# Kernel tuning notes

Measured on AMD Instinct MI355X. Metric: run time of the kernel, lower is better.

Reference implementation:

```python
import jax, jax.numpy as jnp
import numpy as np

V, E, H, D, A, P = 8000, 384, 512, 512, 512, 128
B, N = 16, 128
NEG = -1.0e9


def _lstm(x, Wih, Whh, b, reverse=False):
    # x: (B, T, E); torch gate order i, f, g, o
    Hd = Whh.shape[1]
    def step(carry, xt):
        h, c = carry
        gates = xt @ Wih.T + h @ Whh.T + b
        i, f, g, o = jnp.split(gates, 4, axis=-1)
        c = jax.nn.sigmoid(f) * c + jax.nn.sigmoid(i) * jnp.tanh(g)
        h = jax.nn.sigmoid(o) * jnp.tanh(c)
        return (h, c), h
    xs = jnp.swapaxes(x, 0, 1)
    if reverse:
        xs = xs[::-1]
    init = (jnp.zeros((x.shape[0], Hd), x.dtype), jnp.zeros((x.shape[0], Hd), x.dtype))
    _, hs = jax.lax.scan(step, init, xs)
    if reverse:
        hs = hs[::-1]
    return jnp.swapaxes(hs, 0, 1)


def _forward(src_ids, src_mask, confusionset_mask, emb, Wih_f, Whh_f, b_f, Wih_b, Whh_b, b_b,
             Wih_d, Whh_d, b_d, W1, W2, v_att, combine_W, combine_b, vocab_W, vocab_b,
             Wg_W, Wg_b, ptr_W, ptr_b, ps_W, ps_b):
    x = emb[src_ids]                                                     # (B,N,E)
    # bidirectional encoder
    enc_hs = jnp.concatenate([_lstm(x, Wih_f, Whh_f, b_f),
                              _lstm(x, Wih_b, Whh_b, b_b, reverse=True)], axis=-1)  # (B,N,2H)
    # decoder LSTMCell unrolled over max_len=N steps (teacher forcing on src chars)
    dec_h = _lstm(x, Wih_d, Whh_d, b_d)                                  # (B,N,D)
    # Bahdanau additive attention
    dterm = dec_h @ W1.T                                                 # (B,N,A)
    eterm = enc_hs @ W2.T                                                # (B,N,A)
    score = jnp.tanh(dterm[:, :, None, :] + eterm[:, None, :, :]) @ v_att  # (B,T,n)
    score = jnp.where(src_mask[:, None, :] == 0, NEG, score)
    alpha = jax.nn.softmax(score, axis=-1)
    context = jnp.einsum('btn,bnh->bth', alpha, enc_hs)                  # (B,T,2H)
    combined = jnp.tanh(jnp.concatenate([dec_h, context], axis=-1) @ combine_W.T + combine_b)  # (B,T,D)
    vocab_logits = combined @ vocab_W.T + vocab_b                        # (B,T,V)
    vocab_logits = jnp.where(confusionset_mask == 0, NEG, vocab_logits)
    # pointer logits: Locj = (t == j) indicator as extra feature
    loc = jnp.eye(N, dtype=combined.dtype)                               # (T,n)
    base = combined @ ptr_W[:, :D].T + ptr_b                             # (B,T,P)
    ph = jnp.tanh(base[:, :, None, :] + loc[None, :, :, None] * ptr_W[:, D][None, None, None, :])  # (B,T,n,P)
    pos_scores = ph @ ps_W + ps_b                                        # (B,T,n)
    sentinel = jnp.tanh(combined @ Wg_W.T + Wg_b).sum(-1, keepdims=True) # (B,T,1)
    pointer_logits = jnp.concatenate([pos_scores, sentinel], axis=-1)    # (B,T,n+1)
    pad_mask = jnp.concatenate([src_mask, jnp.ones((src_mask.shape[0], 1), src_mask.dtype)], axis=1)
    pointer_logits = jnp.where(pad_mask[:, None, :] == 0, NEG, pointer_logits)
    return pointer_logits, vocab_logits


def setup_inputs():
    ks = iter(jax.random.split(jax.random.key(0), 40))
    def g(shape, s=0.05):
        return jax.random.normal(next(ks), shape, jnp.float32) * s
    inp = {
        'src_ids': jax.random.randint(next(ks), (B, N), 1, V),
        'src_mask': jnp.ones((B, N), jnp.int32),
        'confusionset_mask': jax.random.randint(next(ks), (B, N, V), 0, 2).astype(jnp.int32),
        'emb': g((V, E)).at[0].set(0.0),  # padding_idx=0 row zeroed
        'Wih_f': g((4 * H, E)), 'Whh_f': g((4 * H, H)), 'b_f': g((4 * H,)),
        'Wih_b': g((4 * H, E)), 'Whh_b': g((4 * H, H)), 'b_b': g((4 * H,)),
        'Wih_d': g((4 * D, E)), 'Whh_d': g((4 * D, D)), 'b_d': g((4 * D,)),
        'W1': g((A, D)), 'W2': g((A, 2 * H)), 'v_att': g((A,)),
        'combine_W': g((D, D + 2 * H)), 'combine_b': g((D,)),
        'vocab_W': g((V, D)), 'vocab_b': g((V,)),
        'Wg_W': g((D, D)), 'Wg_b': g((D,)),
        'ptr_W': g((P, D + 1)), 'ptr_b': g((P,)),
        'ps_W': g((P,)), 'ps_b': g(()),
    }
    return inp


def reference(src_ids, src_mask, confusionset_mask, emb, Wih_f, Whh_f, b_f, Wih_b, Whh_b, b_b,
              Wih_d, Whh_d, b_d, W1, W2, v_att, combine_W, combine_b, vocab_W, vocab_b,
              Wg_W, Wg_b, ptr_W, ptr_b, ps_W, ps_b):
    return _forward(src_ids, src_mask, confusionset_mask, emb, Wih_f, Whh_f, b_f, Wih_b, Whh_b, b_b,
                    Wih_d, Whh_d, b_d, W1, W2, v_att, combine_W, combine_b, vocab_W, vocab_b,
                    Wg_W, Wg_b, ptr_W, ptr_b, ps_W, ps_b)
```

## Files before the change

kernel.cpp:

```cpp
#include <hip/hip_runtime.h>
#include <hip/hip_bf16.h>
#include <math.h>

#define NEGV -1000000000.0f

static constexpr int B_ = 16, N_ = 128, BN_ = 2048;
static constexpr int E_ = 384, V_ = 8000;

typedef __attribute__((ext_vector_type(8))) short short8v;
typedef __attribute__((ext_vector_type(4))) float f32x4;

__device__ inline float wave_sum(float v) {
#pragma unroll
  for (int o = 32; o; o >>= 1) v += __shfl_xor(v, o);
  return v;
}
__device__ inline float wave_max(float v) {
#pragma unroll
  for (int o = 32; o; o >>= 1) v = fmaxf(v, __shfl_xor(v, o));
  return v;
}
__device__ inline float fast_tanh(float x) {
  return 1.f - 2.f / (1.f + __expf(2.f * x));
}
__device__ inline float fast_tanh_pre(float x2) {
  return 1.f - 2.f / (1.f + __expf(x2));
}
__device__ inline float fast_sig(float x) {
  return 1.f / (1.f + __expf(-x));
}
__device__ __forceinline__ void gl16(const void* g, void* l) {
  __builtin_amdgcn_global_load_lds((const __attribute__((address_space(1))) void*)g,
                                   (__attribute__((address_space(3))) void*)l, 16, 0, 0);
}

__global__ __launch_bounds__(256) void embed_kernel(
    const int* __restrict__ ids, const float* __restrict__ emb,
    __hip_bfloat16* __restrict__ xb) {
  const int row = blockIdx.x;
  const int id = ids[row];
  for (int e = threadIdx.x; e < E_; e += 256)
    xb[(size_t)row * E_ + e] = __float2bfloat16(emb[(size_t)id * E_ + e]);
}

struct CastArgs {
  const float* s[12];
  unsigned long long d[12];
  int base[12];
  int total;
  int special;
};
__device__ inline void cast_body(const CastArgs& a, int gsize, int gid0) {
  const int nq = a.total >> 2;
  for (int q = gid0; q < nq; q += gsize) {
    const int e = q << 2;
    int k = 11;
    while (e < a.base[k]) --k;
    const int i = e - a.base[k];
    __hip_bfloat16* dst = (__hip_bfloat16*)a.d[k] + i;
    if (k == a.special) {
      const int row = i >> 9, col = i & 511;
      const float* sp = a.s[k] + (size_t)row * 513 + col;
#pragma unroll
      for (int u = 0; u < 4; ++u) dst[u] = __float2bfloat16(sp[u]);
    } else {
      float4 v = *(const float4*)(a.s[k] + i);
      __hip_bfloat16 h0 = __float2bfloat16(v.x), h1 = __float2bfloat16(v.y);
      __hip_bfloat16 h2 = __float2bfloat16(v.z), h3 = __float2bfloat16(v.w);
      ushort4 u4 = {*(unsigned short*)&h0, *(unsigned short*)&h1,
                    *(unsigned short*)&h2, *(unsigned short*)&h3};
      *(ushort4*)dst = u4;
    }
  }
}
__global__ __launch_bounds__(256) void cast_kernel(CastArgs a) {
  cast_body(a, gridDim.x * 256, blockIdx.x * 256 + threadIdx.x);
}

template <int ACT, bool MASK>
__global__ __launch_bounds__(256) void bgemm_kernel(
    const __hip_bfloat16* __restrict__ A, int lda,
    const __hip_bfloat16* __restrict__ W, int ldw,
    const float* __restrict__ bias,
    float* __restrict__ C, int ldc,
    __hip_bfloat16* __restrict__ Cb, int ldcb,
    int M, int N, int K,
    const int* __restrict__ mask, int ldm) {
  __shared__ __hip_bfloat16 Al[2][4096];
  __shared__ __hip_bfloat16 Bl[2][4096];
  const int tid = threadIdx.x;
  const int wid = tid >> 6, lane = tid & 63;
  const int m0 = blockIdx.y * 128, n0 = blockIdx.x * 128;
  const int nkt = K >> 5;
  const int rm = (wid >> 1) << 6, rn = (wid & 1) << 6;
  const int lrow = lane & 15, kq = lane >> 4;
  const int fs = ((lrow >> 1) & 3) << 4;

  f32x4 acc[4][4];
#pragma unroll
  for (int i = 0; i < 4; ++i)
#pragma unroll
    for (int j = 0; j < 4; ++j) acc[i][j] = {0.f, 0.f, 0.f, 0.f};

  auto stage = [&](int bi, int kt) {
#pragma unroll
    for (int c = 0; c < 2; ++c) {
      const int p = ((c * 4 + wid) << 6) + lane;
      const int row = p >> 2, cb = (p & 3) << 4;
      const int sw = ((row >> 1) & 3) << 4;
      const unsigned loff = (unsigned)__builtin_amdgcn_readfirstlane((c * 4 + wid) << 10);
      {
        const char* src = (const char*)A + ((size_t)(m0 + row) * lda + (size_t)kt * 32) * 2 + (cb ^ sw);
        gl16(src, (char*)&Al[bi][0] + loff);
      }
      {
        int gr = n0 + row;
        if (gr >= N) gr = N - 1;
        const char* src = (const char*)W + ((size_t)gr * ldw + (size_t)kt * 32) * 2 + (cb ^ sw);
        gl16(src, (char*)&Bl[bi][0] + loff);
      }
    }
  };
  auto compute = [&](int bi) {
    const char* Ab = (const char*)&Al[bi][0];
    const char* Bb = (const char*)&Bl[bi][0];
    const int roff = (kq << 4) ^ fs;
    short8v a[4], b[4];
#pragma unroll
    for (int i = 0; i < 4; ++i)
      a[i] = *(const short8v*)(Ab + (rm + i * 16 + lrow) * 64 + roff);
#pragma unroll
    for (int j = 0; j < 4; ++j)
      b[j] = *(const short8v*)(Bb + (rn + j * 16 + lrow) * 64 + roff);
#pragma unroll
    for (int i = 0; i < 4; ++i)
#pragma unroll
      for (int j = 0; j < 4; ++j)
        acc[i][j] = __builtin_amdgcn_mfma_f32_16x16x32_bf16(a[i], b[j], acc[i][j], 0, 0, 0);
  };

  stage(0, 0);
  for (int kt = 0; kt < nkt; ++kt) {
    __syncthreads();
    if (kt + 1 < nkt) stage((kt + 1) & 1, kt + 1);
    compute(kt & 1);
  }

#pragma unroll
  for (int i = 0; i < 4; ++i) {
#pragma unroll
    for (int r = 0; r < 4; ++r) {
      const int m = m0 + rm + i * 16 + kq * 4 + r;
#pragma unroll
      for (int j = 0; j < 4; ++j) {
        const int n = n0 + rn + j * 16 + lrow;
        if (n < N) {
          float v = acc[i][j][r] + (bias ? bias[n] : 0.f);
          if (ACT == 1) v = fast_tanh(v);
          if (MASK) {
            if (mask[(size_t)m * ldm + n] == 0) v = NEGV;
          }
          if (C) C[(size_t)m * ldc + n] = v;
          if (Cb) Cb[(size_t)m * ldcb + n] = __float2bfloat16(v);
        }
      }
    }
  }
}

template <int ACT, int TROUT>
__global__ __launch_bounds__(256) void bgemm64_kernel(
    const __hip_bfloat16* __restrict__ A, int lda,
    const __hip_bfloat16* __restrict__ W, int ldw,
    const float* __restrict__ bias, const float* __restrict__ bias2,
    float* __restrict__ C, int ldc, float* __restrict__ C2,
    __hip_bfloat16* __restrict__ Cb, int ldcb,
    int M, int N, int K,
    long aBs, long wBs, long cBs) {
  __shared__ __hip_bfloat16 Al[2][2048];
  __shared__ __hip_bfloat16 Bl[2][2048];
  A += (size_t)blockIdx.z * aBs;
  W += (size_t)blockIdx.z * wBs;
  const int tid = threadIdx.x;
  const int wid = tid >> 6, lane = tid & 63;
  const int m0 = blockIdx.y * 64, n0 = blockIdx.x * 64;
  const int nkt = K >> 5;
  const int rm = (wid >> 1) << 5, rn = (wid & 1) << 5;
  const int lrow = lane & 15, kq = lane >> 4;
  const int fs = ((lrow >> 1) & 3) << 4;

  f32x4 acc[2][2];
#pragma unroll
  for (int i = 0; i < 2; ++i)
#pragma unroll
    for (int j = 0; j < 2; ++j) acc[i][j] = {0.f, 0.f, 0.f, 0.f};

  auto stage = [&](int bi, int kt) {
    const int p = tid;
    const int row = p >> 2, cb = (p & 3) << 4;
    const int sw = ((row >> 1) & 3) << 4;
    const unsigned loff = (unsigned)__builtin_amdgcn_readfirstlane(wid << 10);
    {
      const char* src = (const char*)A + ((size_t)(m0 + row) * lda + (size_t)kt * 32) * 2 + (cb ^ sw);
      gl16(src, (char*)&Al[bi][0] + loff);
    }
    {
      const char* src = (const char*)W + ((size_t)(n0 + row) * ldw + (size_t)kt * 32) * 2 + (cb ^ sw);
      gl16(src, (char*)&Bl[bi][0] + loff);
    }
  };
  auto compute = [&](int bi) {
    const char* Ab = (const char*)&Al[bi][0];
    const char* Bb = (const char*)&Bl[bi][0];
    const int roff = (kq << 4) ^ fs;
    short8v a[2], b[2];
#pragma unroll
    for (int i = 0; i < 2; ++i)
      a[i] = *(const short8v*)(Ab + (rm + i * 16 + lrow) * 64 + roff);
#pragma unroll
    for (int j = 0; j < 2; ++j)
      b[j] = *(const short8v*)(Bb + (rn + j * 16 + lrow) * 64 + roff);
#pragma unroll
    for (int i = 0; i < 2; ++i)
#pragma unroll
      for (int j = 0; j < 2; ++j)
        acc[i][j] = __builtin_amdgcn_mfma_f32_16x16x32_bf16(a[i], b[j], acc[i][j], 0, 0, 0);
  };

  stage(0, 0);
  for (int kt = 0; kt < nkt; ++kt) {
    __syncthreads();
    if (kt + 1 < nkt) stage((kt + 1) & 1, kt + 1);
    compute(kt & 1);
  }

#pragma unroll
  for (int i = 0; i < 2; ++i) {
#pragma unroll
    for (int r = 0; r < 4; ++r) {
      const int m = m0 + rm + i * 16 + kq * 4 + r;
#pragma unroll
      for (int j = 0; j < 2; ++j) {
        const int n = n0 + rn + j * 16 + lrow;
        float v = acc[i][j][r];
        if (TROUT == 2) {
          if (n < 512) {
            C[(size_t)m * ldc + n] = fast_tanh(v + bias[n]);
          } else {
            C2[(size_t)m * 128 + (n - 512)] = v + bias2[n - 512];
          }
        } else {
          if (ACT == 2) v *= 2.f;
          else {
            v += (bias ? bias[n] : 0.f);
            if (ACT == 1) v = fast_tanh(v);
          }
          if (TROUT == 1) {
            Cb[(((size_t)(m >> 7) * 512 + n) << 7) + (m & 127)] = __float2bfloat16(v);
          } else {
            if (C) C[(size_t)m * ldc + n] = v;
            if (Cb) Cb[(size_t)m * ldcb + n + (size_t)blockIdx.z * cBs] = __float2bfloat16(v);
          }
        }
      }
    }
  }
}

__global__ __launch_bounds__(256) void fused_kernel(
    const __hip_bfloat16* __restrict__ xp16,
    const float* __restrict__ whhF, const float* __restrict__ whhB,
    const float* __restrict__ whhD,
    __hip_bfloat16* __restrict__ hbuf,
    __hip_bfloat16* __restrict__ ehsb, __hip_bfloat16* __restrict__ ehsT,
    __hip_bfloat16* __restrict__ catb,
    CastArgs ca2) {
  extern __shared__ char sm[];
  const int bid = blockIdx.x;
  const int tid = threadIdx.x;

  if (bid >= 96) {
    cast_body(ca2, 64 * 256, (bid - 96) * 256 + tid);
    return;
  }

  const int l = bid >> 5, g = bid & 31;
  const int lane = tid & 63, wid = tid >> 6;
  char* smW = sm;
  char* smH = sm + 65536;
  __hip_bfloat16* hout = (__hip_bfloat16*)(sm + 65536 + 16384);
  char* hist = sm + 65536 + 16384 + 512;

  const float* wsrc = (l == 0) ? whhF : ((l == 1) ? whhB : whhD);
  auto cv = [](float x) -> unsigned {
    __hip_bfloat16 h = __float2bfloat16(x);
    return (unsigned)*(unsigned short*)&h;
  };
  for (int p = tid; p < 4096; p += 256) {
    const int r = p >> 6, cb = (p & 63) << 4;
    const int grow = (r & 3) * 512 + (g << 4) + (r >> 2);
    const float* srcp = wsrc + (size_t)grow * 512 + ((p & 63) << 3);
    float4 u0 = *(const float4*)srcp;
    float4 u1 = *(const float4*)(srcp + 4);
    uint4 q;
    q.x = cv(u0.x) | (cv(u0.y) << 16);
    q.y = cv(u0.z) | (cv(u0.w) << 16);
    q.z = cv(u1.x) | (cv(u1.y) << 16);
    q.w = cv(u1.z) | (cv(u1.w) << 16);
    *(uint4*)(smW + r * 1024 + (cb ^ ((r & 7) << 4))) = q;
  }

  const int lrow = lane & 15, kq = lane >> 4;
  const int swz = (lrow & 7) << 4;
  const char* aB = smW + (wid * 16 + lrow) * 1024;
  const char* bB = smH + lrow * 1024;
  const int dl16 = wid * 4 + kq;
  const int dg = (g << 4) + dl16;
  const int bb = lrow;
  const bool rev = (l == 1);
  const __hip_bfloat16* xl = xp16 + (size_t)l * 2048 * 2048;
  __hip_bfloat16* hb_l = hbuf + (size_t)l * 128 * 8192;
  const int gq = tid >> 3;
  const int b0 = (tid & 7) * 2;
  const int gb = gq * 32;
  const int sw0 = (b0 & 7) << 4, sw1 = ((b0 + 1) & 7) << 4;
  float c = 0.f;

  for (int s = 0; s < 128; ++s) {
    const int t = rev ? 127 - s : s;
    const size_t xro = (size_t)(bb * 128 + t) * 2048 + dg;
    const float xgi = __bfloat162float(xl[xro]);
    const float xgf = __bfloat162float(xl[xro + 512]);
    const float xgg = __bfloat162float(xl[xro + 1024]);
    const float xgo = __bfloat162float(xl[xro + 1536]);

    if (s > 0) {
      if (gq != g) {
        const char* hsrc = (const char*)(hb_l + (size_t)(s - 1) * 8192);
        const unsigned loff = (unsigned)(tid * 64);
        unsigned hv;
        while (true) {
          asm volatile(
              "global_load_ushort %0, %1, %2 sc0 sc1\n\t"
              "s_waitcnt vmcnt(0)"
              : "=&v"(hv) : "v"(loff), "s"(hsrc) : "memory");
          if ((hv & 0xffffu) != 0x7f7fu) break;
          __builtin_amdgcn_s_sleep(1);
        }
        f32x4 q0, q1, q2, q3;
        asm volatile(
            "global_load_dwordx4 %0, %4, %5 sc0 sc1\n\t"
            "global_load_dwordx4 %1, %4, %5 offset:16 sc0 sc1\n\t"
            "global_load_dwordx4 %2, %4, %5 offset:32 sc0 sc1\n\t"
            "global_load_dwordx4 %3, %4, %5 offset:48 sc0 sc1\n\t"
            "s_waitcnt vmcnt(0)"
            : "=&v"(q0), "=&v"(q1), "=&v"(q2), "=&v"(q3)
            : "v"(loff), "s"(hsrc) : "memory");
        *(f32x4*)(smH + b0 * 1024 + (gb ^ sw0)) = q0;
        *(f32x4*)(smH + b0 * 1024 + ((gb + 16) ^ sw0)) = q1;
        *(f32x4*)(smH + (b0 + 1) * 1024 + (gb ^ sw1)) = q2;
        *(f32x4*)(smH + (b0 + 1) * 1024 + ((gb + 16) ^ sw1)) = q3;
      } else {
        const char* hl = (const char*)hout + b0 * 32;
        f32x4 c0 = *(const f32x4*)(hl);
        f32x4 c1 = *(const f32x4*)(hl + 16);
        f32x4 c2 = *(const f32x4*)(hl + 32);
        f32x4 c3 = *(const f32x4*)(hl + 48);
        *(f32x4*)(smH + b0 * 1024 + (gb ^ sw0)) = c0;
        *(f32x4*)(smH + b0 * 1024 + ((gb + 16) ^ sw0)) = c1;
        *(f32x4*)(smH + (b0 + 1) * 1024 + (gb ^ sw1)) = c2;
        *(f32x4*)(smH + (b0 + 1) * 1024 + ((gb + 16) ^ sw1)) = c3;
      }
    } else {
      const f32x4 z = {0.f, 0.f, 0.f, 0.f};
      *(f32x4*)(smH + b0 * 1024 + (gb ^ sw0)) = z;
      *(f32x4*)(smH + b0 * 1024 + ((gb + 16) ^ sw0)) = z;
      *(f32x4*)(smH + (b0 + 1) * 1024 + (gb ^ sw1)) = z;
      *(f32x4*)(smH + (b0 + 1) * 1024 + ((gb + 16) ^ sw1)) = z;
    }
    __syncthreads();

    f32x4 acc0 = {0.f, 0.f, 0.f, 0.f}, acc1 = {0.f, 0.f, 0.f, 0.f};
#pragma unroll
    for (int kt = 0; kt < 16; kt += 2) {
      const int off0 = ((kt * 64 + (kq << 4)) ^ swz);
      const int off1 = (((kt + 1) * 64 + (kq << 4)) ^ swz);
      short8v a0 = *(const short8v*)(aB + off0);
      short8v b0v = *(const short8v*)(bB + off0);
      short8v a1 = *(const short8v*)(aB + off1);
      short8v b1v = *(const short8v*)(bB + off1);
      acc0 = __builtin_amdgcn_mfma_f32_16x16x32_bf16(a0, b0v, acc0, 0, 0, 0);
      acc1 = __builtin_amdgcn_mfma_f32_16x16x32_bf16(a1, b1v, acc1, 0, 0, 0);
    }
    const f32x4 acc = acc0 + acc1;

    const float gi = acc[0] + xgi;
    const float gf = acc[1] + xgf;
    const float gg = acc[2] + xgg;
    const float go = acc[3] + xgo;
    c = fmaf(fast_sig(gf), c, fast_sig(gi) * fast_tanh(gg));
    const float h = fast_sig(go) * fast_tanh(c);
    __hip_bfloat16 hb16 = __float2bfloat16(h);
    const unsigned short hraw = *(unsigned short*)&hb16;
    hout[bb * 16 + dl16] = hb16;
    *(unsigned short*)(hist + s * 512 + (bb * 16 + dl16) * 2) = hraw;
    __syncthreads();

    if (s < 127 && wid == (s & 3) && (lane < 32)) {
      f32x4 hv4 = *(const f32x4*)((const char*)hout + lane * 16);
      char* hdst = (char*)(hb_l + (size_t)s * 8192);
      asm volatile("global_store_dwordx4 %0, %1, %2 sc0 sc1"
                   :: "v"((unsigned)((g << 9) + lane * 16)), "v"(hv4), "s"(hdst)
                   : "memory");
    }
  }

  __syncthreads();
  const int bb2 = tid >> 4, lo2 = tid & 15;
  if (l < 2) {
    const int hoff = (bb2 * 16 + lo2) * 2;
    char* dstT = (char*)(ehsT + ((size_t)bb2 * 1024 + l * 512 + (g << 4) + lo2) * 128);
    for (int tc = 0; tc < 128; tc += 32) {
      unsigned v[16];
#pragma unroll
      for (int w = 0; w < 16; ++w) {
        const int t0 = tc + 2 * w;
        const int s0 = rev ? 127 - t0 : t0;
        const int s1 = rev ? 126 - t0 : t0 + 1;
        unsigned a = *(const unsigned short*)(hist + s0 * 512 + hoff);
        unsigned b2 = *(const unsigned short*)(hist + s1 * 512 + hoff);
        v[w] = a | (b2 << 16);
      }
#pragma unroll
      for (int q = 0; q < 4; ++q)
        *(uint4*)(dstT + tc * 2 + q * 16) =
            make_uint4(v[q * 4], v[q * 4 + 1], v[q * 4 + 2], v[q * 4 + 3]);
    }
    for (int k = 0; k < 8; ++k) {
      const int t = lo2 * 8 + k;
      const int s0 = rev ? 127 - t : t;
      const char* srcp = hist + s0 * 512 + bb2 * 32;
      uint4 ra = *(const uint4*)srcp;
      uint4 rb = *(const uint4*)(srcp + 16);
      char* dp = (char*)(ehsb + ((size_t)(bb2 * 128 + t)) * 1024 + l * 512 + (g << 4));
      *(uint4*)dp = ra;
      *(uint4*)(dp + 16) = rb;
    }
  } else {
    for (int k = 0; k < 8; ++k) {
      const int t = lo2 * 8 + k;
      const char* srcp = hist + t * 512 + bb2 * 32;
      uint4 ra = *(const uint4*)srcp;
      uint4 rb = *(const uint4*)(srcp + 16);
      char* dp = (char*)(catb + ((size_t)(bb2 * 128 + t)) * 1536 + (g << 4));
      *(uint4*)dp = ra;
      *(uint4*)(dp + 16) = rb;
    }
  }
}

__global__ __launch_bounds__(256) void score_kernel(
    const float* __restrict__ dterm, const __hip_bfloat16* __restrict__ etT,
    const float* __restrict__ v_att, const int* __restrict__ src_mask,
    __hip_bfloat16* __restrict__ alphab) {
  const int b = blockIdx.x >> 5, tg = blockIdx.x & 31;
  const int t0 = tg * 4;
  const int tid = threadIdx.x;
  __shared__ float dt[4][512], vs[512], red[4][4][128], al[4][128];
  for (int i = tid; i < 2048; i += 256)
    dt[i >> 9][i & 511] = dterm[((size_t)(b * 128 + t0 + (i >> 9))) * 512 + (i & 511)];
  vs[tid] = v_att[tid];
  vs[tid + 256] = v_att[256 + tid];
  __syncthreads();
  const int n0 = (tid & 63) << 1, ah = tid >> 6;
  {
    const __hip_bfloat16* ep = etT + (((size_t)b * 512 + ah * 128) << 7) + n0;
    const float* vp = vs + ah * 128;
    const float* dp0 = &dt[0][ah * 128];
    const float* dp1 = &dt[1][ah * 128];
    const float* dp2 = &dt[2][ah * 128];
    const float* dp3 = &dt[3][ah * 128];
    float p00 = 0, p01 = 0, p10 = 0, p11 = 0, p20 = 0, p21 = 0, p30 = 0, p31 = 0;
    for (int a = 0; a < 128; ++a) {
      const unsigned u = *(const unsigned*)(ep + ((size_t)a << 7));
      unsigned u0 = u << 16, u1 = u & 0xffff0000u;
      const float e0 = __builtin_bit_cast(float, u0);
      const float e1 = __builtin_bit_cast(float, u1);
      const float va = vp[a];
      p00 = fmaf(va, fast_tanh_pre(dp0[a] + e0), p00);
      p01 = fmaf(va, fast_tanh_pre(dp0[a] + e1), p01);
      p10 = fmaf(va, fast_tanh_pre(dp1[a] + e0), p10);
      p11 = fmaf(va, fast_tanh_pre(dp1[a] + e1), p11);
      p20 = fmaf(va, fast_tanh_pre(dp2[a] + e0), p20);
      p21 = fmaf(va, fast_tanh_pre(dp2[a] + e1), p21);
      p30 = fmaf(va, fast_tanh_pre(dp3[a] + e0), p30);
      p31 = fmaf(va, fast_tanh_pre(dp3[a] + e1), p31);
    }
    red[0][ah][n0] = p00; red[0][ah][n0 + 1] = p01;
    red[1][ah][n0] = p10; red[1][ah][n0 + 1] = p11;
    red[2][ah][n0] = p20; red[2][ah][n0 + 1] = p21;
    red[3][ah][n0] = p30; red[3][ah][n0 + 1] = p31;
  }
  __syncthreads();
#pragma unroll
  for (int tp = 0; tp < 2; ++tp) {
    const int tt = tp * 2 + (tid >> 7);
    const int n = tid & 127;
    float sc = red[tt][0][n] + red[tt][1][n] + red[tt][2][n] + red[tt][3][n];
    if (src_mask[b * 128 + n] == 0) sc = NEGV;
    al[tt][n] = sc;
  }
  __syncthreads();
  {
    const int tt = tid >> 6, lane = tid & 63;
    const float v0 = al[tt][lane], v1 = al[tt][lane + 64];
    const float m = wave_max(fmaxf(v0, v1));
    const float e0 = __expf(v0 - m), e1 = __expf(v1 - m);
    const float inv = 1.f / wave_sum(e0 + e1);
    __hip_bfloat16* ap = alphab + ((size_t)(b * 128 + t0 + tt)) * 128;
    ap[lane] = __float2bfloat16(e0 * inv);
    ap[lane + 64] = __float2bfloat16(e1 * inv);
  }
}

__global__ __launch_bounds__(256) void pointer_kernel(
    const float* __restrict__ base, const float* __restrict__ wgout,
    const float* __restrict__ ptr_W, const float* __restrict__ ps_W,
    const float* __restrict__ ps_b, const int* __restrict__ src_mask,
    float* __restrict__ out0) {
  const int bt = blockIdx.x;
  const int b = bt >> 7, t = bt & 127;
  const int tid = threadIdx.x;
  __shared__ float r0[4], r1[4], r2[4], fin[3];
  float off_p = 0.f, diag_p = 0.f, sent_p;
  if (tid < 128) {
    const float ba = base[(size_t)bt * 128 + tid];
    const float pw = ps_W[tid];
    off_p = tanhf(ba) * pw;
    diag_p = tanhf(ba + ptr_W[tid * 513 + 512]) * pw;
  }
  sent_p = wgout[(size_t)bt * 512 + tid] + wgout[(size_t)bt * 512 + 256 + tid];
  off_p = wave_sum(off_p);
  diag_p = wave_sum(diag_p);
  sent_p = wave_sum(sent_p);
  const int wid = tid >> 6, lane = tid & 63;
  if (lane == 0) { r0[wid] = off_p; r1[wid] = diag_p; r2[wid] = sent_p; }
  __syncthreads();
  if (tid == 0) {
    const float psb = ps_b[0];
    fin[0] = r0[0] + r0[1] + r0[2] + r0[3] + psb;
    fin[1] = r1[0] + r1[1] + r1[2] + r1[3] + psb;
    fin[2] = r2[0] + r2[1] + r2[2] + r2[3];
  }
  __syncthreads();
  const float s_off = fin[0], s_diag = fin[1], sent = fin[2];
  if (tid < 129) {
    float v;
    if (tid == 128) v = sent;
    else {
      v = (tid == t) ? s_diag : s_off;
      if (src_mask[b * 128 + tid] == 0) v = NEGV;
    }
    out0[(size_t)bt * 129 + tid] = v;
  }
}

extern "C" void kernel_launch(void* const* d_in, const int* in_sizes, int n_in,
                              void* d_out, int out_size, void* d_ws, size_t ws_size,
                              hipStream_t stream) {
  const int* src_ids   = (const int*)d_in[0];
  const int* src_mask  = (const int*)d_in[1];
  const int* cmask     = (const int*)d_in[2];
  const float* emb     = (const float*)d_in[3];
  const float* Wih_f   = (const float*)d_in[4];
  const float* Whh_f   = (const float*)d_in[5];
  const float* b_f     = (const float*)d_in[6];
  const float* Wih_b   = (const float*)d_in[7];
  const float* Whh_b   = (const float*)d_in[8];
  const float* b_b     = (const float*)d_in[9];
  const float* Wih_d   = (const float*)d_in[10];
  const float* Whh_d   = (const float*)d_in[11];
  const float* b_d     = (const float*)d_in[12];
  const float* W1      = (const float*)d_in[13];
  const float* W2      = (const float*)d_in[14];
  const float* v_att   = (const float*)d_in[15];
  const float* comb_W  = (const float*)d_in[16];
  const float* comb_b  = (const float*)d_in[17];
  const float* vocab_W = (const float*)d_in[18];
  const float* vocab_b = (const float*)d_in[19];
  const float* Wg_W    = (const float*)d_in[20];
  const float* Wg_b    = (const float*)d_in[21];
  const float* ptr_W   = (const float*)d_in[22];
  const float* ptr_b   = (const float*)d_in[23];
  const float* ps_W    = (const float*)d_in[24];
  const float* ps_b    = (const float*)d_in[25];
  (void)in_sizes; (void)n_in; (void)out_size; (void)ws_size;

  char* wsb = (char*)d_ws;
  size_t o = 0;
  auto alloc = [&](size_t bytes) { char* p = wsb + o; o = (o + bytes + 255) & ~(size_t)255; return p; };
  __hip_bfloat16* xb      = (__hip_bfloat16*)alloc((size_t)BN_ * E_ * 2);
  __hip_bfloat16* xproj16 = (__hip_bfloat16*)alloc((size_t)3 * BN_ * 2048 * 2);
  __hip_bfloat16* ehsb    = (__hip_bfloat16*)alloc((size_t)BN_ * 1024 * 2);
  __hip_bfloat16* ehsT    = (__hip_bfloat16*)alloc((size_t)16 * 1024 * 128 * 2);
  __hip_bfloat16* catb    = (__hip_bfloat16*)alloc((size_t)BN_ * 1536 * 2);
  float* dterm            = (float*)alloc((size_t)BN_ * 512 * 4);
  __hip_bfloat16* etT     = (__hip_bfloat16*)alloc((size_t)16 * 512 * 128 * 2);
  __hip_bfloat16* alphab  = (__hip_bfloat16*)alloc((size_t)BN_ * 128 * 2);
  __hip_bfloat16* combb   = (__hip_bfloat16*)alloc((size_t)BN_ * 512 * 2);
  float* wgout            = (float*)alloc((size_t)BN_ * 512 * 4);
  float* baseb            = (float*)alloc((size_t)BN_ * 128 * 4);
  __hip_bfloat16* hbuf    = (__hip_bfloat16*)alloc((size_t)3 * 128 * 8192 * 2);
  __hip_bfloat16* wihf16  = (__hip_bfloat16*)alloc((size_t)2048 * 384 * 2);
  __hip_bfloat16* wihb16  = (__hip_bfloat16*)alloc((size_t)2048 * 384 * 2);
  __hip_bfloat16* wihd16  = (__hip_bfloat16*)alloc((size_t)2048 * 384 * 2);
  __hip_bfloat16* w1_16   = (__hip_bfloat16*)alloc((size_t)512 * 512 * 2);
  __hip_bfloat16* w2_16   = (__hip_bfloat16*)alloc((size_t)512 * 1024 * 2);
  __hip_bfloat16* combw16 = (__hip_bfloat16*)alloc((size_t)512 * 1536 * 2);
  __hip_bfloat16* vocw16  = (__hip_bfloat16*)alloc((size_t)8000 * 512 * 2);
  __hip_bfloat16* wgw16   = (__hip_bfloat16*)alloc((size_t)512 * 512 * 2);
  __hip_bfloat16* ptrw16  = (__hip_bfloat16*)alloc((size_t)128 * 512 * 2);

  float* out0 = (float*)d_out;
  float* out1 = out0 + (size_t)BN_ * 129;

  hipError_t e0 = hipMemsetAsync(hbuf, 0x7f, (size_t)3 * 128 * 8192 * 2, stream);
  (void)e0;
  embed_kernel<<<BN_, 256, 0, stream>>>(src_ids, emb, xb);

  CastArgs c1;
  {
    const float* s3[3] = {Wih_f, Wih_b, Wih_d};
    __hip_bfloat16* d3[3] = {wihf16, wihb16, wihd16};
    int acc = 0;
    for (int k = 0; k < 3; ++k) {
      c1.s[k] = s3[k]; c1.d[k] = (unsigned long long)d3[k]; c1.base[k] = acc;
      acc += 2048 * 384;
    }
    for (int k = 3; k < 12; ++k) { c1.s[k] = nullptr; c1.d[k] = 0; c1.base[k] = 0x7fffffff; }
    c1.total = acc; c1.special = -1;
  }
  cast_kernel<<<1024, 256, 0, stream>>>(c1);

  bgemm_kernel<0, false><<<dim3(16, 16), 256, 0, stream>>>(
      xb, E_, wihf16, E_, b_f, nullptr, 0, xproj16, 2048, BN_, 2048, E_, nullptr, 0);
  bgemm_kernel<0, false><<<dim3(16, 16), 256, 0, stream>>>(
      xb, E_, wihb16, E_, b_b, nullptr, 0, xproj16 + (size_t)BN_ * 2048, 2048, BN_, 2048, E_, nullptr, 0);
  bgemm_kernel<0, false><<<dim3(16, 16), 256, 0, stream>>>(
      xb, E_, wihd16, E_, b_d, nullptr, 0, xproj16 + (size_t)2 * BN_ * 2048, 2048, BN_, 2048, E_, nullptr, 0);

  CastArgs c2;
  {
    const float* s6[6] = {W1, W2, comb_W, vocab_W, Wg_W, ptr_W};
    __hip_bfloat16* d6[6] = {w1_16, w2_16, combw16, vocw16, wgw16, ptrw16};
    int ns[6] = {512 * 512, 512 * 1024, 512 * 1536, 8000 * 512, 512 * 512, 128 * 512};
    int acc = 0;
    for (int k = 0; k < 6; ++k) {
      c2.s[k] = s6[k]; c2.d[k] = (unsigned long long)d6[k]; c2.base[k] = acc;
      acc += ns[k];
    }
    for (int k = 6; k < 12; ++k) { c2.s[k] = nullptr; c2.d[k] = 0; c2.base[k] = 0x7fffffff; }
    c2.total = acc; c2.special = 5;
  }

  hipError_t e1 = hipFuncSetAttribute((const void*)fused_kernel,
                      hipFuncAttributeMaxDynamicSharedMemorySize, 147968);
  (void)e1;
  fused_kernel<<<160, 256, 147968, stream>>>(
      xproj16, Whh_f, Whh_b, Whh_d, hbuf, ehsb, ehsT, catb, c2);

  bgemm64_kernel<2, 0><<<dim3(8, 32), 256, 0, stream>>>(
      catb, 1536, w1_16, 512, nullptr, nullptr, dterm, 512, nullptr, nullptr, 0,
      BN_, 512, 512, 0, 0, 0);
  bgemm64_kernel<2, 1><<<dim3(8, 32), 256, 0, stream>>>(
      ehsb, 1024, w2_16, 1024, nullptr, nullptr, nullptr, 0, nullptr, etT, 0,
      BN_, 512, 1024, 0, 0, 0);

  score_kernel<<<16 * 32, 256, 0, stream>>>(dterm, etT, v_att, src_mask, alphab);

  bgemm64_kernel<0, 0><<<dim3(16, 2, 16), 256, 0, stream>>>(
      alphab, 128, ehsT, 128, nullptr, nullptr, nullptr, 0, nullptr,
      catb + 512, 1536, 128, 1024, 128, 128 * 128, 1024 * 128, 128 * 1536);

  bgemm64_kernel<1, 0><<<dim3(8, 32), 256, 0, stream>>>(
      catb, 1536, combw16, 1536, comb_b, nullptr, nullptr, 0, nullptr,
      combb, 512, BN_, 512, 1536, 0, 0, 0);

  bgemm_kernel<0, true><<<dim3(63, 16), 256, 0, stream>>>(
      combb, 512, vocw16, 512, vocab_b, out1, V_, nullptr, 0, BN_, V_, 512, cmask, V_);

  bgemm64_kernel<0, 2><<<dim3(10, 32), 256, 0, stream>>>(
      combb, 512, wgw16, 512, Wg_b, ptr_b, wgout, 512, baseb, nullptr, 0,
      BN_, 640, 512, 0, 0, 0);

  pointer_kernel<<<BN_, 256, 0, stream>>>(baseb, wgout, ptr_W, ps_W, ps_b, src_mask, out0);
}
```

Baseline: 605.6 us.

## Merge prologue, projection and tail GEMM launches into fewer combined kernels

The memset of hbuf, the embedding gather and the Wih weight cast are folded into one prologue kernel that splits its work by block index. The memset becomes cache-bypassing stores of the 0x7f pattern. The three input-projection GEMMs become one launch with a z dimension. The two attention projection GEMMs are merged into one launch, and so are the vocab and Wg/pointer GEMMs, by dispatching on block id. The GEMM bodies are turned into device functions with runtime activation and output modes. This removes several kernel launches and the gaps between them, and lets independent GEMMs share one grid. The cost is some branching and fewer compile-time specialisations.

```diff
diff --git a/kernel.cpp b/kernel.cpp
--- a/kernel.cpp
+++ b/kernel.cpp
@@ -34,19 +34,10 @@
                                    (__attribute__((address_space(3))) void*)l, 16, 0, 0);
 }
 
-__global__ __launch_bounds__(256) void embed_kernel(
-    const int* __restrict__ ids, const float* __restrict__ emb,
-    __hip_bfloat16* __restrict__ xb) {
-  const int row = blockIdx.x;
-  const int id = ids[row];
-  for (int e = threadIdx.x; e < E_; e += 256)
-    xb[(size_t)row * E_ + e] = __float2bfloat16(emb[(size_t)id * E_ + e]);
-}
-
 struct CastArgs {
-  const float* s[12];
-  unsigned long long d[12];
-  int base[12];
+  const float* s[6];
+  unsigned long long d[6];
+  int base[6];
   int total;
   int special;
 };
@@ -54,7 +45,7 @@
   const int nq = a.total >> 2;
   for (int q = gid0; q < nq; q += gsize) {
     const int e = q << 2;
-    int k = 11;
+    int k = 5;
     while (e < a.base[k]) --k;
     const int i = e - a.base[k];
     __hip_bfloat16* dst = (__hip_bfloat16*)a.d[k] + i;
@@ -73,24 +64,41 @@
     }
   }
 }
-__global__ __launch_bounds__(256) void cast_kernel(CastArgs a) {
-  cast_body(a, gridDim.x * 256, blockIdx.x * 256 + threadIdx.x);
+
+__global__ __launch_bounds__(256) void prologue_kernel(
+    const int* __restrict__ ids, const float* __restrict__ emb,
+    __hip_bfloat16* __restrict__ xb, __hip_bfloat16* __restrict__ hbuf,
+    CastArgs c1) {
+  const int bid = blockIdx.x, tid = threadIdx.x;
+  if (bid < 256) {
+    for (int row = bid; row < 2048; row += 256) {
+      const int id = ids[row];
+      for (int e = tid; e < E_; e += 256)
+        xb[(size_t)row * E_ + e] = __float2bfloat16(emb[(size_t)id * E_ + e]);
+    }
+  } else if (bid < 288) {
+    const unsigned total = 3u * 128u * 8192u * 2u;
+    const float pf = __builtin_bit_cast(float, 0x7f7f7f7fu);
+    f32x4 pat = {pf, pf, pf, pf};
+    char* base = (char*)hbuf;
+    for (unsigned off = (unsigned)((bid - 256) * 256 + tid) * 16u; off < total;
+         off += 32u * 256u * 16u) {
+      asm volatile("global_store_dwordx4 %0, %1, %2 sc0 sc1"
+                   :: "v"(off), "v"(pat), "s"(base) : "memory");
+    }
+  } else {
+    cast_body(c1, 256 * 256, (bid - 288) * 256 + tid);
+  }
 }
 
 template <int ACT, bool MASK>
-__global__ __launch_bounds__(256) void bgemm_kernel(
-    const __hip_bfloat16* __restrict__ A, int lda,
-    const __hip_bfloat16* __restrict__ W, int ldw,
-    const float* __restrict__ bias,
-    float* __restrict__ C, int ldc,
-    __hip_bfloat16* __restrict__ Cb, int ldcb,
-    int M, int N, int K,
-    const int* __restrict__ mask, int ldm) {
-  __shared__ __hip_bfloat16 Al[2][4096];
-  __shared__ __hip_bfloat16 Bl[2][4096];
+__device__ __forceinline__ void gemm128_impl(
+    const __hip_bfloat16* A, int lda, const __hip_bfloat16* W, int ldw,
+    const float* bias, float* C, int ldc, __hip_bfloat16* Cb, int ldcb,
+    int N, int K, const int* mask, int ldm, int m0, int n0,
+    __hip_bfloat16 (*Al)[4096], __hip_bfloat16 (*Bl)[4096]) {
   const int tid = threadIdx.x;
   const int wid = tid >> 6, lane = tid & 63;
-  const int m0 = blockIdx.y * 128, n0 = blockIdx.x * 128;
   const int nkt = K >> 5;
   const int rm = (wid >> 1) << 6, rn = (wid & 1) << 6;
   const int lrow = lane & 15, kq = lane >> 4;
@@ -168,22 +176,13 @@
   }
 }
 
-template <int ACT, int TROUT>
-__global__ __launch_bounds__(256) void bgemm64_kernel(
-    const __hip_bfloat16* __restrict__ A, int lda,
-    const __hip_bfloat16* __restrict__ W, int ldw,
-    const float* __restrict__ bias, const float* __restrict__ bias2,
-    float* __restrict__ C, int ldc, float* __restrict__ C2,
-    __hip_bfloat16* __restrict__ Cb, int ldcb,
-    int M, int N, int K,
-    long aBs, long wBs, long cBs) {
-  __shared__ __hip_bfloat16 Al[2][2048];
-  __shared__ __hip_bfloat16 Bl[2][2048];
-  A += (size_t)blockIdx.z * aBs;
-  W += (size_t)blockIdx.z * wBs;
+__device__ __forceinline__ void gemm64_impl(
+    const __hip_bfloat16* A, int lda, const __hip_bfloat16* W, int ldw,
+    const float* bias, const float* bias2,
+    float* C, int ldc, float* C2, __hip_bfloat16* Cb, int ldcb,
+    int K, int act, int trout, int m0, int n0, char* AlB, char* BlB) {
   const int tid = threadIdx.x;
   const int wid = tid >> 6, lane = tid & 63;
-  const int m0 = blockIdx.y * 64, n0 = blockIdx.x * 64;
   const int nkt = K >> 5;
   const int rm = (wid >> 1) << 5, rn = (wid & 1) << 5;
   const int lrow = lane & 15, kq = lane >> 4;
@@ -196,22 +195,21 @@
     for (int j = 0; j < 2; ++j) acc[i][j] = {0.f, 0.f, 0.f, 0.f};
 
   auto stage = [&](int bi, int kt) {
-    const int p = tid;
-    const int row = p >> 2, cb = (p & 3) << 4;
+    const int row = tid >> 2, cb = (tid & 3) << 4;
     const int sw = ((row >> 1) & 3) << 4;
     const unsigned loff = (unsigned)__builtin_amdgcn_readfirstlane(wid << 10);
     {
       const char* src = (const char*)A + ((size_t)(m0 + row) * lda + (size_t)kt * 32) * 2 + (cb ^ sw);
-      gl16(src, (char*)&Al[bi][0] + loff);
+      gl16(src, AlB + bi * 4096 + loff);
     }
     {
       const char* src = (const char*)W + ((size_t)(n0 + row) * ldw + (size_t)kt * 32) * 2 + (cb ^ sw);
-      gl16(src, (char*)&Bl[bi][0] + loff);
+      gl16(src, BlB + bi * 4096 + loff);
     }
   };
   auto compute = [&](int bi) {
-    const char* Ab = (const char*)&Al[bi][0];
-    const char* Bb = (const char*)&Bl[bi][0];
+    const char* Ab = AlB + bi * 4096;
+    const char* Bb = BlB + bi * 4096;
     const int roff = (kq << 4) ^ fs;
     short8v a[2], b[2];
 #pragma unroll
@@ -243,27 +241,98 @@
       for (int j = 0; j < 2; ++j) {
         const int n = n0 + rn + j * 16 + lrow;
         float v = acc[i][j][r];
-        if (TROUT == 2) {
+        if (trout == 2) {
           if (n < 512) {
             C[(size_t)m * ldc + n] = fast_tanh(v + bias[n]);
           } else {
             C2[(size_t)m * 128 + (n - 512)] = v + bias2[n - 512];
           }
         } else {
-          if (ACT == 2) v *= 2.f;
+          if (act == 2) v *= 2.f;
           else {
             v += (bias ? bias[n] : 0.f);
-            if (ACT == 1) v = fast_tanh(v);
+            if (act == 1) v = fast_tanh(v);
           }
-          if (TROUT == 1) {
+          if (trout == 1) {
             Cb[(((size_t)(m >> 7) * 512 + n) << 7) + (m & 127)] = __float2bfloat16(v);
           } else {
             if (C) C[(size_t)m * ldc + n] = v;
-            if (Cb) Cb[(size_t)m * ldcb + n + (size_t)blockIdx.z * cBs] = __float2bfloat16(v);
+            if (Cb) Cb[(size_t)m * ldcb + n] = __float2bfloat16(v);
           }
         }
       }
     }
+  }
+}
+
+__global__ __launch_bounds__(256) void xproj_kernel(
+    const __hip_bfloat16* __restrict__ A, const __hip_bfloat16* __restrict__ Wih,
+    const float* __restrict__ b0, const float* __restrict__ b1,
+    const float* __restrict__ b2, __hip_bfloat16* __restrict__ xproj16) {
+  __shared__ __hip_bfloat16 Al[2][4096], Bl[2][4096];
+  const int z = blockIdx.z;
+  const float* bias = (z == 0) ? b0 : (z == 1 ? b1 : b2);
+  gemm128_impl<0, false>(A, E_, Wih + (size_t)z * 2048 * 384, E_, bias,
+                         nullptr, 0, xproj16 + (size_t)z * BN_ * 2048, 2048,
+                         2048, E_, nullptr, 0, blockIdx.y * 128,
+                         blockIdx.x * 128, Al, Bl);
+}
+
+__global__ __launch_bounds__(256) void qk_kernel(
+    const __hip_bfloat16* __restrict__ catb, const __hip_bfloat16* __restrict__ ehsb,
+    const __hip_bfloat16* __restrict__ w1, const __hip_bfloat16* __restrict__ w2,
+    float* __restrict__ dterm, __hip_bfloat16* __restrict__ etT) {
+  __shared__ char AlB[8192], BlB[8192];
+  const int bid = blockIdx.x;
+  if (bid < 256) {
+    const int bx = bid & 7, by = bid >> 3;
+    gemm64_impl(catb, 1536, w1, 512, nullptr, nullptr, dterm, 512, nullptr,
+                nullptr, 0, 512, 2, 0, by * 64, bx * 64, AlB, BlB);
+  } else {
+    const int l = bid - 256;
+    const int bx = l & 7, by = l >> 3;
+    gemm64_impl(ehsb, 1024, w2, 1024, nullptr, nullptr, nullptr, 0, nullptr,
+                etT, 0, 1024, 2, 1, by * 64, bx * 64, AlB, BlB);
+  }
+}
+
+__global__ __launch_bounds__(256) void ctx_kernel(
+    const __hip_bfloat16* __restrict__ alphab, const __hip_bfloat16* __restrict__ ehsT,
+    __hip_bfloat16* __restrict__ catbCtx) {
+  __shared__ char AlB[8192], BlB[8192];
+  const int z = blockIdx.z;
+  gemm64_impl(alphab + (size_t)z * 128 * 128, 128,
+              ehsT + (size_t)z * 1024 * 128, 128, nullptr, nullptr, nullptr, 0,
+              nullptr, catbCtx + (size_t)z * 128 * 1536, 1536, 128, 0, 0,
+              blockIdx.y * 64, blockIdx.x * 64, AlB, BlB);
+}
+
+__global__ __launch_bounds__(256) void comb_kernel(
+    const __hip_bfloat16* __restrict__ catb, const __hip_bfloat16* __restrict__ combw,
+    const float* __restrict__ comb_b, __hip_bfloat16* __restrict__ combb) {
+  __shared__ char AlB[8192], BlB[8192];
+  gemm64_impl(catb, 1536, combw, 1536, comb_b, nullptr, nullptr, 0, nullptr,
+              combb, 512, 1536, 1, 0, blockIdx.y * 64, blockIdx.x * 64, AlB, BlB);
+}
+
+__global__ __launch_bounds__(256) void tail_kernel(
+    const __hip_bfloat16* __restrict__ combb, const __hip_bfloat16* __restrict__ vocw,
+    const float* __restrict__ vocab_b, float* __restrict__ out1,
+    const int* __restrict__ cmask,
+    const __hip_bfloat16* __restrict__ wgw, const float* __restrict__ Wg_b,
+    const float* __restrict__ ptr_b, float* __restrict__ wgout,
+    float* __restrict__ baseb) {
+  __shared__ __hip_bfloat16 Al[2][4096], Bl[2][4096];
+  const int bid = blockIdx.x;
+  if (bid < 1008) {
+    const int bx = bid % 63, by = bid / 63;
+    gemm128_impl<0, true>(combb, 512, vocw, 512, vocab_b, out1, V_, nullptr, 0,
+                          V_, 512, cmask, V_, by * 128, bx * 128, Al, Bl);
+  } else {
+    const int l = bid - 1008;
+    const int bx = l % 10, by = l / 10;
+    gemm64_impl(combb, 512, wgw, 512, Wg_b, ptr_b, wgout, 512, baseb, nullptr,
+                0, 512, 0, 2, by * 64, bx * 64, (char*)Al, (char*)Bl);
   }
 }
 
@@ -611,9 +680,7 @@
   float* wgout            = (float*)alloc((size_t)BN_ * 512 * 4);
   float* baseb            = (float*)alloc((size_t)BN_ * 128 * 4);
   __hip_bfloat16* hbuf    = (__hip_bfloat16*)alloc((size_t)3 * 128 * 8192 * 2);
-  __hip_bfloat16* wihf16  = (__hip_bfloat16*)alloc((size_t)2048 * 384 * 2);
-  __hip_bfloat16* wihb16  = (__hip_bfloat16*)alloc((size_t)2048 * 384 * 2);
-  __hip_bfloat16* wihd16  = (__hip_bfloat16*)alloc((size_t)2048 * 384 * 2);
+  __hip_bfloat16* wih16   = (__hip_bfloat16*)alloc((size_t)3 * 2048 * 384 * 2);
   __hip_bfloat16* w1_16   = (__hip_bfloat16*)alloc((size_t)512 * 512 * 2);
   __hip_bfloat16* w2_16   = (__hip_bfloat16*)alloc((size_t)512 * 1024 * 2);
   __hip_bfloat16* combw16 = (__hip_bfloat16*)alloc((size_t)512 * 1536 * 2);
@@ -624,31 +691,19 @@
   float* out0 = (float*)d_out;
   float* out1 = out0 + (size_t)BN_ * 129;
 
-  hipError_t e0 = hipMemsetAsync(hbuf, 0x7f, (size_t)3 * 128 * 8192 * 2, stream);
-  (void)e0;
-  embed_kernel<<<BN_, 256, 0, stream>>>(src_ids, emb, xb);
-
   CastArgs c1;
   {
     const float* s3[3] = {Wih_f, Wih_b, Wih_d};
-    __hip_bfloat16* d3[3] = {wihf16, wihb16, wihd16};
     int acc = 0;
     for (int k = 0; k < 3; ++k) {
-      c1.s[k] = s3[k]; c1.d[k] = (unsigned long long)d3[k]; c1.base[k] = acc;
+      c1.s[k] = s3[k];
+      c1.d[k] = (unsigned long long)(wih16 + (size_t)k * 2048 * 384);
+      c1.base[k] = acc;
       acc += 2048 * 384;
     }
-    for (int k = 3; k < 12; ++k) { c1.s[k] = nullptr; c1.d[k] = 0; c1.base[k] = 0x7fffffff; }
+    for (int k = 3; k < 6; ++k) { c1.s[k] = nullptr; c1.d[k] = 0; c1.base[k] = 0x7fffffff; }
     c1.total = acc; c1.special = -1;
   }
-  cast_kernel<<<1024, 256, 0, stream>>>(c1);
-
-  bgemm_kernel<0, false><<<dim3(16, 16), 256, 0, stream>>>(
-      xb, E_, wihf16, E_, b_f, nullptr, 0, xproj16, 2048, BN_, 2048, E_, nullptr, 0);
-  bgemm_kernel<0, false><<<dim3(16, 16), 256, 0, stream>>>(
-      xb, E_, wihb16, E_, b_b, nullptr, 0, xproj16 + (size_t)BN_ * 2048, 2048, BN_, 2048, E_, nullptr, 0);
-  bgemm_kernel<0, false><<<dim3(16, 16), 256, 0, stream>>>(
-      xb, E_, wihd16, E_, b_d, nullptr, 0, xproj16 + (size_t)2 * BN_ * 2048, 2048, BN_, 2048, E_, nullptr, 0);
-
   CastArgs c2;
   {
     const float* s6[6] = {W1, W2, comb_W, vocab_W, Wg_W, ptr_W};
@@ -659,9 +714,13 @@
       c2.s[k] = s6[k]; c2.d[k] = (unsigned long long)d6[k]; c2.base[k] = acc;
       acc += ns[k];
     }
-    for (int k = 6; k < 12; ++k) { c2.s[k] = nullptr; c2.d[k] = 0; c2.base[k] = 0x7fffffff; }
     c2.total = acc; c2.special = 5;
   }
+
+  prologue_kernel<<<544, 256, 0, stream>>>(src_ids, emb, xb, hbuf, c1);
+
+  xproj_kernel<<<dim3(16, 16, 3), 256, 0, stream>>>(
+      xb, wih16, b_f, b_b, b_d, xproj16);
 
   hipError_t e1 = hipFuncSetAttribute((const void*)fused_kernel,
                       hipFuncAttributeMaxDynamicSharedMemorySize, 147968);
@@ -669,29 +728,16 @@
   fused_kernel<<<160, 256, 147968, stream>>>(
       xproj16, Whh_f, Whh_b, Whh_d, hbuf, ehsb, ehsT, catb, c2);
 
-  bgemm64_kernel<2, 0><<<dim3(8, 32), 256, 0, stream>>>(
-      catb, 1536, w1_16, 512, nullptr, nullptr, dterm, 512, nullptr, nullptr, 0,
-      BN_, 512, 512, 0, 0, 0);
-  bgemm64_kernel<2, 1><<<dim3(8, 32), 256, 0, stream>>>(
-      ehsb, 1024, w2_16, 1024, nullptr, nullptr, nullptr, 0, nullptr, etT, 0,
-      BN_, 512, 1024, 0, 0, 0);
+  qk_kernel<<<512, 256, 0, stream>>>(catb, ehsb, w1_16, w2_16, dterm, etT);
 
   score_kernel<<<16 * 32, 256, 0, stream>>>(dterm, etT, v_att, src_mask, alphab);
 
-  bgemm64_kernel<0, 0><<<dim3(16, 2, 16), 256, 0, stream>>>(
-      alphab, 128, ehsT, 128, nullptr, nullptr, nullptr, 0, nullptr,
-      catb + 512, 1536, 128, 1024, 128, 128 * 128, 1024 * 128, 128 * 1536);
-
-  bgemm64_kernel<1, 0><<<dim3(8, 32), 256, 0, stream>>>(
-      catb, 1536, combw16, 1536, comb_b, nullptr, nullptr, 0, nullptr,
-      combb, 512, BN_, 512, 1536, 0, 0, 0);
-
-  bgemm_kernel<0, true><<<dim3(63, 16), 256, 0, stream>>>(
-      combb, 512, vocw16, 512, vocab_b, out1, V_, nullptr, 0, BN_, V_, 512, cmask, V_);
-
-  bgemm64_kernel<0, 2><<<dim3(10, 32), 256, 0, stream>>>(
-      combb, 512, wgw16, 512, Wg_b, ptr_b, wgout, 512, baseb, nullptr, 0,
-      BN_, 640, 512, 0, 0, 0);
+  ctx_kernel<<<dim3(16, 2, 16), 256, 0, stream>>>(alphab, ehsT, catb + 512);
+
+  comb_kernel<<<dim3(8, 32), 256, 0, stream>>>(catb, combw16, comb_b, combb);
+
+  tail_kernel<<<1328, 256, 0, stream>>>(combb, vocw16, vocab_b, out1, cmask,
+                                        wgw16, Wg_b, ptr_b, wgout, baseb);
 
   pointer_kernel<<<BN_, 256, 0, stream>>>(baseb, wgout, ptr_W, ps_W, ps_b, src_mask, out0);
 }
```

Result: faster. 586.6 us (-3.1%).
